# Kernel tuning notes

Hardware: AMD Instinct MI355X
Metric: run time of the kernel (lower is better)

## Reference

```python
import jax, jax.numpy as jnp
import numpy as np

B, C, H, W = 2, 1024, 64, 64
E, TOP_K = 8, 2
FFN = C  # ffn_dim = in_channels; hidden_dim = out_channels = in_channels


def setup_inputs() -> dict:
    key = jax.random.key(0)
    ks = jax.random.split(key, 5)
    s = 0.02
    return {
        "hidden_states": jax.random.normal(ks[0], (B, C, H, W), jnp.float32),
        "gate_w": jax.random.normal(ks[1], (E, C), jnp.float32) * s,   # torch Linear weight [out,in]
        "w1": jax.random.normal(ks[2], (E, FFN, C), jnp.float32) * s,
        "w2": jax.random.normal(ks[3], (E, C, FFN), jnp.float32) * s,
        "w3": jax.random.normal(ks[4], (E, FFN, C), jnp.float32) * s,
    }


def reference(hidden_states, gate_w, w1, w2, w3):
    b, c = hidden_states.shape[0], hidden_states.shape[1]
    space = hidden_states.shape[2:]
    # (B, C, H, W) -> (B, H, W, C) -> (T, C)
    x = jnp.transpose(hidden_states, (0, 2, 3, 1)).reshape(-1, c)

    # Router: softmax in float32, top-k, renormalize (matches torch)
    logits = x @ gate_w.T                                   # [T, E]
    probs = jax.nn.softmax(logits.astype(jnp.float32), axis=-1)
    rw, sel = jax.lax.top_k(probs, TOP_K)                   # [T, K]
    rw = rw / jnp.sum(rw, axis=-1, keepdims=True)
    rw = rw.astype(x.dtype)

    # Combine weights per expert: zero where expert not selected -> exact
    # equivalence with gather/scatter dispatch (full capacity, no drops).
    combine = jnp.sum(jax.nn.one_hot(sel, E, dtype=x.dtype) * rw[..., None], axis=1)  # [T, E]

    out = jnp.zeros_like(x)
    for e in range(E):  # small fixed expert loop
        h = jax.nn.gelu(x @ w1[e].T, approximate=False) * (x @ w3[e].T)  # SwiGLU-style [T, FFN]
        out = out + combine[:, e:e + 1] * (h @ w2[e].T)

    out = out.reshape(b, *space, c)
    return jnp.transpose(out, (0, 3, 1, 2))  # (B, C, H, W)
```

## Files before the change

### kernel.cpp

```cpp
#include <hip/hip_runtime.h>
#include <hip/hip_bf16.h>
#include <math.h>

#define BB 2
#define CC 1024
#define HH 64
#define WW 64
#define HWH (HH*WW)
#define TT (BB*HWH)
#define EE 8
#define FFN 1024
#define MAXTILES 71
#define HCAP (MAXTILES*256)

typedef __bf16 bf16x8 __attribute__((ext_vector_type(8)));
typedef __bf16 bf16x4 __attribute__((ext_vector_type(4)));
typedef float  f32x4  __attribute__((ext_vector_type(4)));

__device__ __forceinline__ void gl_lds16(const __bf16* g, __bf16* l) {
    __builtin_amdgcn_global_load_lds(
        (const __attribute__((address_space(1))) void*)g,
        (__attribute__((address_space(3))) void*)l, 16, 0, 0);
}

__device__ __forceinline__ void barrier_raw() {
    asm volatile("" ::: "memory");
    __builtin_amdgcn_s_barrier();
    asm volatile("" ::: "memory");
}

#define WAITV(N) asm volatile("s_waitcnt vmcnt(" #N ")" ::: "memory")
#define LGKM0()  asm volatile("s_waitcnt lgkmcnt(0)" ::: "memory")

#define MFMA16(ACC, AF, BF)                                                   \
    _Pragma("unroll") for (int m_ = 0; m_ < 4; ++m_)                          \
    _Pragma("unroll") for (int n_ = 0; n_ < 4; ++n_)                          \
        ACC[m_][n_] = __builtin_amdgcn_mfma_f32_16x16x32_bf16(                \
            AF[m_], BF[n_], ACC[m_][n_], 0, 0, 0);

#define CVB 12288
#define XPB 8192
#define RTB 512
__global__ __launch_bounds__(256) void k_prep(
    const float* __restrict__ hs, const float* __restrict__ gate_w,
    const float* __restrict__ w1, const float* __restrict__ w2,
    const float* __restrict__ w3,
    __bf16* __restrict__ w1b, __bf16* __restrict__ w2b,
    __bf16* __restrict__ w3b, __bf16* __restrict__ X,
    float* __restrict__ logP) {
    __shared__ float sm[2112];
    const int bid = blockIdx.x;
    const int tid = threadIdx.x;

    if (bid < CVB) {
        const float* s; __bf16* d; int lb = bid;
        if (lb < 4096)      { s = w1; d = w1b; }
        else if (lb < 8192) { s = w2; d = w2b; lb -= 4096; }
        else                { s = w3; d = w3b; lb -= 8192; }
        const size_t i = (size_t)lb * 2048 + (size_t)tid * 8;
        const f32x4 v0 = *(const f32x4*)&s[i];
        const f32x4 v1 = *(const f32x4*)&s[i + 4];
        bf16x8 o;
#pragma unroll
        for (int j = 0; j < 4; ++j) { o[j] = (__bf16)v0[j]; o[4 + j] = (__bf16)v1[j]; }
        *(bf16x8*)&d[i] = o;
    } else if (bid < CVB + XPB) {
        const int lb  = bid - CVB;
        const int hw0 = (lb & 127) * 32;
        const int c0  = ((lb >> 7) & 31) * 32;
        const int b   = lb >> 12;
        float (*tile)[33] = (float(*)[33])sm;
        const int tx = tid & 31, ty = tid >> 5;
        const float* src = hs + ((size_t)b * CC + c0) * HWH + hw0;
#pragma unroll
        for (int i = 0; i < 4; ++i)
            tile[ty + i * 8][tx] = src[(size_t)(ty + i * 8) * HWH + tx];
        __syncthreads();
        __bf16* dst = X + ((size_t)b * HWH + hw0) * CC + c0;
#pragma unroll
        for (int i = 0; i < 4; ++i) {
            const int hwl = ty + i * 8;
            dst[(size_t)hwl * CC + tx] = (__bf16)tile[tx][hwl];
        }
    } else {
        const int lb  = bid - (CVB + XPB);
        const int q   = lb & 3;
        const int t64 = lb >> 2;
        float* g = sm;
        for (int i = tid; i < 2048; i += 256)
            g[i] = gate_w[(size_t)(i >> 8) * CC + q * 256 + (i & 255)];
        __syncthreads();
        const int q2 = tid >> 6, tl = tid & 63;
        const int t  = t64 * 64 + tl;
        const int b  = t >> 12, hw = t & 4095;
        const float* xp = hs + (size_t)b * CC * HWH + hw;
        float l[EE];
#pragma unroll
        for (int e = 0; e < EE; ++e) l[e] = 0.0f;
        const int cbase = q * 256 + q2 * 64;
        for (int c2 = 0; c2 < 64; ++c2) {
            const float xv = xp[(size_t)(cbase + c2) * HWH];
#pragma unroll
            for (int e = 0; e < EE; ++e) l[e] += xv * g[e * 256 + q2 * 64 + c2];
        }
        float* dst = logP + ((size_t)(q * 4 + q2) * TT + t) * 8;
        f32x4 a, c;
#pragma unroll
        for (int e = 0; e < 4; ++e) { a[e] = l[e]; c[e] = l[4 + e]; }
        *(f32x4*)dst = a;
        *(f32x4*)&dst[4] = c;
    }
}

__global__ __launch_bounds__(256) void k_top2(const float* __restrict__ logP,
                                              int* __restrict__ cnt,
                                              int* __restrict__ idxl,
                                              int* __restrict__ tokE,
                                              int* __restrict__ tokP,
                                              float* __restrict__ tokW) {
    __shared__ int lcnt[EE], lbase[EE];
    const int tid = threadIdx.x;
    const int t   = blockIdx.x * 256 + tid;
    if (tid < EE) lcnt[tid] = 0;
    __syncthreads();

    float l[EE];
#pragma unroll
    for (int e = 0; e < EE; ++e) l[e] = 0.0f;
#pragma unroll
    for (int pq = 0; pq < 16; ++pq) {
        const float* src = logP + ((size_t)pq * TT + t) * 8;
        const f32x4 a = *(const f32x4*)src;
        const f32x4 c = *(const f32x4*)&src[4];
#pragma unroll
        for (int e = 0; e < 4; ++e) { l[e] += a[e]; l[4 + e] += c[e]; }
    }

    int e1 = 0; float v1 = l[0];
#pragma unroll
    for (int e = 1; e < EE; ++e) { if (l[e] > v1) { v1 = l[e]; e1 = e; } }
    int e2 = -1; float v2 = -1e30f;
#pragma unroll
    for (int e = 0; e < EE; ++e) { if (e != e1 && l[e] > v2) { v2 = l[e]; e2 = e; } }

    const float p2 = __expf(v2 - v1);
    const float rs = 1.0f / (1.0f + p2);

    const int m1 = atomicAdd(&lcnt[e1], 1);
    const int m2 = atomicAdd(&lcnt[e2], 1);
    __syncthreads();
    if (tid < EE) lbase[tid] = atomicAdd(&cnt[tid], lcnt[tid]);
    __syncthreads();
    const int p1pos = lbase[e1] + m1;
    const int p2pos = lbase[e2] + m2;

    idxl[e1 * TT + p1pos] = t;
    idxl[e2 * TT + p2pos] = t;
    tokE[t] = e1 | (e2 << 8);
    tokP[2 * t]     = p1pos;
    tokP[2 * t + 1] = p2pos;
    tokW[2 * t]     = rs;
    tokW[2 * t + 1] = p2 * rs;
}

__global__ void k_offsets(const int* __restrict__ cnt, int* __restrict__ off,
                          int* __restrict__ tileE, int* __restrict__ tileM,
                          int* __restrict__ nT) {
    if (threadIdx.x == 0) {
        int a = 0, n = 0;
        for (int e = 0; e < EE; ++e) {
            off[e] = a;
            const int mt = (cnt[e] + 255) >> 8;
            for (int m = 0; m < mt; ++m) { tileE[n] = e; tileM[n] = m * 256; ++n; }
            a += mt * 256;
        }
        nT[0] = n;
    }
}

__global__ __launch_bounds__(512, 2)
void k_gemm1(const __bf16* __restrict__ X, const __bf16* __restrict__ w1b,
             const __bf16* __restrict__ w3b, const int* __restrict__ cnt,
             const int* __restrict__ off, const int* __restrict__ idxl,
             const int* __restrict__ tileE, const int* __restrict__ tileM,
             const int* __restrict__ nT, __bf16* __restrict__ H) {
    if ((int)blockIdx.y >= nT[0]) return;
    const int e    = tileE[blockIdx.y];
    const int mt   = tileM[blockIdx.y];
    const int cntE = cnt[e];
    const int goff = off[e];
    const int n0   = blockIdx.x * 128;
    const __bf16* W1 = w1b + (size_t)e * FFN * CC;
    const __bf16* W3 = w3b + (size_t)e * FFN * CC;

    __shared__ __align__(16) __bf16 sA[4][256 * 32];
    __shared__ __align__(16) __bf16 sB1[4][128 * 32];
    __shared__ __align__(16) __bf16 sB3[4][128 * 32];

    const int tid  = threadIdx.x;
    const int lane = tid & 63, wave = tid >> 6;
    const int l15  = lane & 15, lq = (lane >> 4) & 3;
    const int wm   = (wave >> 1) * 64;
    const int wn   = (wave & 1) * 64;
    const int cs   = (lq ^ (l15 & 3)) * 8;
    const int r_l  = tid >> 2;
    const int csw8 = ((tid & 3) ^ (r_l & 3)) * 8;

    int p0 = mt + r_l;        if (p0 > cntE - 1) p0 = cntE - 1;
    int p1 = mt + 128 + r_l;  if (p1 > cntE - 1) p1 = cntE - 1;
    const __bf16* gA0 = X + (size_t)idxl[e * TT + p0] * CC + csw8;
    const __bf16* gA1 = X + (size_t)idxl[e * TT + p1] * CC + csw8;
    const __bf16* gW1 = W1 + (size_t)(n0 + r_l) * CC + csw8;
    const __bf16* gW3 = W3 + (size_t)(n0 + r_l) * CC + csw8;

    const int aoff = (wm + l15) * 32 + cs;
    const int boff = (wn + l15) * 32 + cs;
    const int dA   = wave * 512;

    f32x4 acc1[4][4] = {};
    f32x4 acc3[4][4] = {};

#define STG1A(S, KT) do { const int kb_ = (KT) * 32;                          \
        gl_lds16(gA0 + kb_, &sA[S][dA]);                                      \
        gl_lds16(gA1 + kb_, &sA[S][4096 + dA]); } while (0)
#define STG1B(S, KT) do { const int kb_ = (KT) * 32;                          \
        gl_lds16(gW1 + kb_, &sB1[S][dA]);                                     \
        gl_lds16(gW3 + kb_, &sB3[S][dA]); } while (0)

    STG1A(0, 0); STG1B(0, 0);
    STG1A(1, 1); STG1B(1, 1);
    STG1A(2, 2); STG1B(2, 2);
    WAITV(8);
    barrier_raw();

#define TILE1(KT, S, PREF, WN) do {                                           \
    bf16x8 af_[4], bf_[4];                                                    \
    _Pragma("unroll") for (int i_ = 0; i_ < 4; ++i_) {                        \
        af_[i_] = *(const bf16x8*)&sA[S][aoff + i_ * 512];                    \
        bf_[i_] = *(const bf16x8*)&sB1[S][boff + i_ * 512];                   \
    }                                                                         \
    if (PREF) STG1A((S + 3) & 3, (KT) + 3);                                   \
    barrier_raw();                                                            \
    LGKM0();                                                                  \
    __builtin_amdgcn_s_setprio(1);                                            \
    MFMA16(acc1, af_, bf_);                                                   \
    __builtin_amdgcn_s_setprio(0);                                            \
    barrier_raw();                                                            \
    _Pragma("unroll") for (int i_ = 0; i_ < 4; ++i_)                          \
        bf_[i_] = *(const bf16x8*)&sB3[S][boff + i_ * 512];                   \
    if (PREF) STG1B((S + 3) & 3, (KT) + 3);                                   \
    barrier_raw();                                                            \
    LGKM0();                                                                  \
    __builtin_amdgcn_s_setprio(1);                                            \
    MFMA16(acc3, af_, bf_);                                                   \
    __builtin_amdgcn_s_setprio(0);                                            \
    WAITV(WN);                                                                \
    barrier_raw();                                                            \
} while (0)

    for (int k4 = 0; k4 < 28; k4 += 4) {
        TILE1(k4 + 0, 0, 1, 8);
        TILE1(k4 + 1, 1, 1, 8);
        TILE1(k4 + 2, 2, 1, 8);
        TILE1(k4 + 3, 3, 1, 8);
    }
    TILE1(28, 0, 1, 8);
    TILE1(29, 1, 0, 4);
    TILE1(30, 2, 0, 0);
    TILE1(31, 3, 0, 63);

#pragma unroll
    for (int m = 0; m < 4; ++m) {
        const int gb = goff + mt + wm + m * 16 + lq * 4;
#pragma unroll
        for (int n = 0; n < 4; ++n) {
            const int nb = n0 + wn + n * 16 + l15;
#pragma unroll
            for (int r = 0; r < 4; ++r) {
                const float a  = acc1[m][n][r];
                const float c  = acc3[m][n][r];
                const float ge = 0.5f * a * (1.0f + erff(a * 0.70710678118654752f));
                H[(size_t)(gb + r) * FFN + nb] = (__bf16)(ge * c);
            }
        }
    }
}

__global__ __launch_bounds__(512, 2)
void k_gemm2(const __bf16* __restrict__ H, const __bf16* __restrict__ w2b,
             const int* __restrict__ off, const int* __restrict__ tileE,
             const int* __restrict__ tileM, const int* __restrict__ nT,
             __bf16* __restrict__ Z) {
    if ((int)blockIdx.y >= nT[0]) return;
    const int e    = tileE[blockIdx.y];
    const int mt   = tileM[blockIdx.y];
    const int goff = off[e];
    const int n0   = blockIdx.x * 256;
    const __bf16* W2 = w2b + (size_t)e * CC * FFN;
    const __bf16* Ar = H + (size_t)(goff + mt) * FFN;

    __shared__ __align__(16) __bf16 sA[4][256 * 32];
    __shared__ __align__(16) __bf16 sB[4][256 * 32];

    const int tid  = threadIdx.x;
    const int lane = tid & 63, wave = tid >> 6;
    const int l15  = lane & 15, lq = (lane >> 4) & 3;
    const int wm   = (wave & 1) * 128;
    const int wn   = (wave >> 1) * 64;
    const int cs   = (lq ^ (l15 & 3)) * 8;
    const int r_l  = tid >> 2;
    const int csw8 = ((tid & 3) ^ (r_l & 3)) * 8;

    const __bf16* gA0 = Ar + (size_t)r_l * FFN + csw8;
    const __bf16* gA1 = Ar + (size_t)(128 + r_l) * FFN + csw8;
    const __bf16* gB0 = W2 + (size_t)(n0 + r_l) * FFN + csw8;
    const __bf16* gB1 = W2 + (size_t)(n0 + 128 + r_l) * FFN + csw8;

    const int aoff = (wm + l15) * 32 + cs;
    const int boff = (wn + l15) * 32 + cs;
    const int dA   = wave * 512;

    f32x4 accL[4][4] = {};
    f32x4 accH[4][4] = {};

#define STG2A(S, KT) do { const int kb_ = (KT) * 32;                          \
        gl_lds16(gA0 + kb_, &sA[S][dA]);                                      \
        gl_lds16(gA1 + kb_, &sA[S][4096 + dA]); } while (0)
#define STG2B(S, KT) do { const int kb_ = (KT) * 32;                          \
        gl_lds16(gB0 + kb_, &sB[S][dA]);                                      \
        gl_lds16(gB1 + kb_, &sB[S][4096 + dA]); } while (0)

    STG2A(0, 0); STG2B(0, 0);
    STG2A(1, 1); STG2B(1, 1);
    STG2A(2, 2); STG2B(2, 2);
    WAITV(8);
    barrier_raw();

#define TILE2(KT, S, PREF, WN) do {                                           \
    bf16x8 af_[4], bf_[4];                                                    \
    _Pragma("unroll") for (int i_ = 0; i_ < 4; ++i_) {                        \
        af_[i_] = *(const bf16x8*)&sA[S][aoff + i_ * 512];                    \
        bf_[i_] = *(const bf16x8*)&sB[S][boff + i_ * 512];                    \
    }                                                                         \
    if (PREF) STG2A((S + 3) & 3, (KT) + 3);                                   \
    barrier_raw();                                                            \
    LGKM0();                                                                  \
    __builtin_amdgcn_s_setprio(1);                                            \
    MFMA16(accL, af_, bf_);                                                   \
    __builtin_amdgcn_s_setprio(0);                                            \
    barrier_raw();                                                            \
    _Pragma("unroll") for (int i_ = 0; i_ < 4; ++i_)                          \
        af_[i_] = *(const bf16x8*)&sA[S][aoff + 2048 + i_ * 512];             \
    if (PREF) STG2B((S + 3) & 3, (KT) + 3);                                   \
    barrier_raw();                                                            \
    LGKM0();                                                                  \
    __builtin_amdgcn_s_setprio(1);                                            \
    MFMA16(accH, af_, bf_);                                                   \
    __builtin_amdgcn_s_setprio(0);                                            \
    WAITV(WN);                                                                \
    barrier_raw();                                                            \
} while (0)

    for (int k4 = 0; k4 < 28; k4 += 4) {
        TILE2(k4 + 0, 0, 1, 8);
        TILE2(k4 + 1, 1, 1, 8);
        TILE2(k4 + 2, 2, 1, 8);
        TILE2(k4 + 3, 3, 1, 8);
    }
    TILE2(28, 0, 1, 8);
    TILE2(29, 1, 0, 4);
    TILE2(30, 2, 0, 0);
    TILE2(31, 3, 0, 63);

#pragma unroll
    for (int m = 0; m < 4; ++m) {
#pragma unroll
        for (int n = 0; n < 4; ++n) {
            const int nb = n0 + wn + n * 16 + l15;
#pragma unroll
            for (int r = 0; r < 4; ++r) {
                Z[(size_t)(goff + mt + wm + m * 16 + lq * 4 + r) * CC + nb] =
                    (__bf16)accL[m][n][r];
                Z[(size_t)(goff + mt + wm + 64 + m * 16 + lq * 4 + r) * CC + nb] =
                    (__bf16)accH[m][n][r];
            }
        }
    }
}

__global__ __launch_bounds__(256) void k_combine(const __bf16* __restrict__ Z,
                                                 const int* __restrict__ off,
                                                 const int* __restrict__ tokE,
                                                 const int* __restrict__ tokP,
                                                 const float* __restrict__ tokW,
                                                 float* __restrict__ out) {
    __shared__ float tile[32][33];
    const int t0 = blockIdx.x * 32;
    const int c0 = blockIdx.y * 32;
    const int tx = threadIdx.x & 31;
    const int ty = threadIdx.x >> 5;

#pragma unroll
    for (int i = 0; i < 4; ++i) {
        const int tl = ty + 8 * i;
        const int t  = t0 + tl;
        const int ee = tokE[t];
        const int e1 = ee & 0xff, e2 = ee >> 8;
        const int r1 = off[e1] + tokP[2 * t];
        const int r2 = off[e2] + tokP[2 * t + 1];
        const float v = tokW[2 * t]     * (float)Z[(size_t)r1 * CC + c0 + tx]
                      + tokW[2 * t + 1] * (float)Z[(size_t)r2 * CC + c0 + tx];
        tile[tl][tx] = v;
    }
    __syncthreads();

    const int b   = t0 >> 12;
    const int hw0 = t0 & 4095;
#pragma unroll
    for (int i = 0; i < 4; ++i) {
        const int cl = ty + 8 * i;
        out[(size_t)b * CC * HWH + (size_t)(c0 + cl) * HWH + hw0 + tx] = tile[tx][cl];
    }
}

extern "C" void kernel_launch(void* const* d_in, const int* in_sizes, int n_in,
                              void* d_out, int out_size, void* d_ws, size_t ws_size,
                              hipStream_t stream) {
    const float* hs     = (const float*)d_in[0];
    const float* gate_w = (const float*)d_in[1];
    const float* w1     = (const float*)d_in[2];
    const float* w2     = (const float*)d_in[3];
    const float* w3     = (const float*)d_in[4];
    float* out = (float*)d_out;

    const size_t WSZ = (size_t)EE * FFN * CC * 2;
    char* ws = (char*)d_ws;
    __bf16* w2b  = (__bf16*)ws;
    __bf16* w1b  = (__bf16*)(ws + WSZ);
    __bf16* w3b  = (__bf16*)(ws + 2 * WSZ);
    __bf16* X    = (__bf16*)(ws + 3 * WSZ);
    __bf16* Zbuf = (__bf16*)(ws + WSZ);
    __bf16* Hbuf = (__bf16*)(ws + 4 * WSZ);
    float*  logP = (float*)Hbuf;
    char* p = ws + 4 * WSZ + (size_t)HCAP * FFN * 2;
    int*   idxl  = (int*)p;           p += (size_t)EE * TT * 4;
    int*   tokE  = (int*)p;           p += (size_t)TT * 4;
    int*   tokP  = (int*)p;           p += (size_t)2 * TT * 4;
    float* tokW  = (float*)p;         p += (size_t)2 * TT * 4;
    int*   cnt   = (int*)p;           p += 256;
    int*   off   = (int*)p;           p += 256;
    int*   tileE = (int*)p;           p += MAXTILES * 4;
    int*   tileM = (int*)p;           p += MAXTILES * 4;
    int*   nT    = (int*)p;

    hipMemsetAsync(cnt, 0, EE * sizeof(int), stream);

    k_prep<<<CVB + XPB + RTB, 256, 0, stream>>>(
        hs, gate_w, w1, w2, w3, w1b, w2b, w3b, X, logP);
    k_top2<<<TT / 256, 256, 0, stream>>>(logP, cnt, idxl, tokE, tokP, tokW);
    k_offsets<<<1, 64, 0, stream>>>(cnt, off, tileE, tileM, nT);

    k_gemm1<<<dim3(FFN / 128, MAXTILES), 512, 0, stream>>>(
        X, w1b, w3b, cnt, off, idxl, tileE, tileM, nT, Hbuf);
    k_gemm2<<<dim3(CC / 256, MAXTILES), 512, 0, stream>>>(
        Hbuf, w2b, off, tileE, tileM, nT, Zbuf);
    k_combine<<<dim3(TT / 32, CC / 32), 256, 0, stream>>>(
        Zbuf, off, tokE, tokP, tokW, out);
}
```

Measured before the change: 383.5 us.

## Restructure MoE GEMM kernels to double-buffered BK=64 with 128x64 wave tiles

Both expert GEMM kernels move from a 4-stage BK=32 pipeline to a 2-stage double buffer that covers 64 of K per stage. Each wave now owns a 128x64 output subtile, with 8x4 accumulators and interleaved W1/W3 columns in gemm1. The LDS swizzle pattern changes and sched_barrier hints are added. Launch bounds drop to one block per CU to free registers for the larger accumulator set, at the cost of lower occupancy and less latency hiding.

```diff
diff --git a/kernel.cpp b/kernel.cpp
--- a/kernel.cpp
+++ b/kernel.cpp
@@ -14,7 +14,6 @@
 #define HCAP (MAXTILES*256)
 
 typedef __bf16 bf16x8 __attribute__((ext_vector_type(8)));
-typedef __bf16 bf16x4 __attribute__((ext_vector_type(4)));
 typedef float  f32x4  __attribute__((ext_vector_type(4)));
 
 __device__ __forceinline__ void gl_lds16(const __bf16* g, __bf16* l) {
@@ -31,12 +30,9 @@
 
 #define WAITV(N) asm volatile("s_waitcnt vmcnt(" #N ")" ::: "memory")
 #define LGKM0()  asm volatile("s_waitcnt lgkmcnt(0)" ::: "memory")
-
-#define MFMA16(ACC, AF, BF)                                                   \
-    _Pragma("unroll") for (int m_ = 0; m_ < 4; ++m_)                          \
-    _Pragma("unroll") for (int n_ = 0; n_ < 4; ++n_)                          \
-        ACC[m_][n_] = __builtin_amdgcn_mfma_f32_16x16x32_bf16(                \
-            AF[m_], BF[n_], ACC[m_][n_], 0, 0, 0);
+#define SCHED0() __builtin_amdgcn_sched_barrier(0)
+#define PRIO1()  __builtin_amdgcn_s_setprio(1)
+#define PRIO0()  __builtin_amdgcn_s_setprio(0)
 
 #define CVB 12288
 #define XPB 8192
@@ -178,7 +174,7 @@
     }
 }
 
-__global__ __launch_bounds__(512, 2)
+__global__ __launch_bounds__(512, 1)
 void k_gemm1(const __bf16* __restrict__ X, const __bf16* __restrict__ w1b,
              const __bf16* __restrict__ w3b, const int* __restrict__ cnt,
              const int* __restrict__ off, const int* __restrict__ idxl,
@@ -193,100 +189,114 @@
     const __bf16* W1 = w1b + (size_t)e * FFN * CC;
     const __bf16* W3 = w3b + (size_t)e * FFN * CC;
 
-    __shared__ __align__(16) __bf16 sA[4][256 * 32];
-    __shared__ __align__(16) __bf16 sB1[4][128 * 32];
-    __shared__ __align__(16) __bf16 sB3[4][128 * 32];
+    __shared__ __align__(16) __bf16 sA[2][2][256 * 32];
+    __shared__ __align__(16) __bf16 sB[2][2][256 * 32];
 
     const int tid  = threadIdx.x;
     const int lane = tid & 63, wave = tid >> 6;
-    const int l15  = lane & 15, lq = (lane >> 4) & 3;
-    const int wm   = (wave >> 1) * 64;
-    const int wn   = (wave & 1) * 64;
-    const int cs   = (lq ^ (l15 & 3)) * 8;
-    const int r_l  = tid >> 2;
-    const int csw8 = ((tid & 3) ^ (r_l & 3)) * 8;
-
-    int p0 = mt + r_l;        if (p0 > cntE - 1) p0 = cntE - 1;
-    int p1 = mt + 128 + r_l;  if (p1 > cntE - 1) p1 = cntE - 1;
-    const __bf16* gA0 = X + (size_t)idxl[e * TT + p0] * CC + csw8;
-    const __bf16* gA1 = X + (size_t)idxl[e * TT + p1] * CC + csw8;
-    const __bf16* gW1 = W1 + (size_t)(n0 + r_l) * CC + csw8;
-    const __bf16* gW3 = W3 + (size_t)(n0 + r_l) * CC + csw8;
-
-    const int aoff = (wm + l15) * 32 + cs;
-    const int boff = (wn + l15) * 32 + cs;
-    const int dA   = wave * 512;
-
-    f32x4 acc1[4][4] = {};
-    f32x4 acc3[4][4] = {};
-
-#define STG1A(S, KT) do { const int kb_ = (KT) * 32;                          \
-        gl_lds16(gA0 + kb_, &sA[S][dA]);                                      \
-        gl_lds16(gA1 + kb_, &sA[S][4096 + dA]); } while (0)
-#define STG1B(S, KT) do { const int kb_ = (KT) * 32;                          \
-        gl_lds16(gW1 + kb_, &sB1[S][dA]);                                     \
-        gl_lds16(gW3 + kb_, &sB3[S][dA]); } while (0)
-
-    STG1A(0, 0); STG1B(0, 0);
-    STG1A(1, 1); STG1B(1, 1);
-    STG1A(2, 2); STG1B(2, 2);
-    WAITV(8);
+    const int l15  = lane & 15, lq = lane >> 4;
+    const int wm   = wave & 1;
+    const int q    = wave >> 1;
+    const int rsw  = (lq ^ ((l15 >> 1) & 3)) * 8;
+
+    const int rl  = lane >> 2;
+    const int csw = ((lane & 3) ^ ((rl >> 1) & 3)) * 8;
+
+    int pr0 = mt + wave * 32 + rl;       if (pr0 > cntE - 1) pr0 = cntE - 1;
+    int pr1 = mt + wave * 32 + 16 + rl;  if (pr1 > cntE - 1) pr1 = cntE - 1;
+    const __bf16* gA0 = X + (size_t)idxl[e * TT + pr0] * CC + csw;
+    const __bf16* gA1 = X + (size_t)idxl[e * TT + pr1] * CC + csw;
+    const __bf16* WB = (wave & 1) ? W3 : W1;
+    const __bf16* gB0 = WB + (size_t)(n0 + q * 32 + rl) * CC + csw;
+    const __bf16* gB1 = WB + (size_t)(n0 + q * 32 + 16 + rl) * CC + csw;
+
+    const int st0  = wave * 1024;
+    const int aoff = (wm * 128 + l15) * 32 + rsw;
+    const int boff = (q * 64 + l15) * 32 + rsw;
+
+    f32x4 acc[8][4] = {};
+
+#define G1_STGA(S, KS, KB) do {                                               \
+    gl_lds16(gA0 + (KB) + (KS) * 32, &sA[S][KS][st0]);                        \
+    gl_lds16(gA1 + (KB) + (KS) * 32, &sA[S][KS][st0 + 512]); } while (0)
+#define G1_STGB(S, KS, KB) do {                                               \
+    gl_lds16(gB0 + (KB) + (KS) * 32, &sB[S][KS][st0]);                        \
+    gl_lds16(gB1 + (KB) + (KS) * 32, &sB[S][KS][st0 + 512]); } while (0)
+#define G1_LDA(DST, S, KS, MF0)                                               \
+    _Pragma("unroll") for (int mf_ = 0; mf_ < 4; ++mf_)                       \
+        DST[mf_] = *(const bf16x8*)&sA[S][KS][aoff + (MF0 + mf_) * 512];
+#define G1_LDB(DST, S, KS)                                                    \
+    _Pragma("unroll") for (int nf_ = 0; nf_ < 4; ++nf_)                       \
+        DST[nf_] = *(const bf16x8*)&sB[S][KS][boff + nf_ * 512];
+#define G1_MM(M0, AF, BF)                                                     \
+    _Pragma("unroll") for (int m_ = 0; m_ < 4; ++m_)                          \
+    _Pragma("unroll") for (int n_ = 0; n_ < 4; ++n_)                          \
+        acc[M0 + m_][n_] = __builtin_amdgcn_mfma_f32_16x16x32_bf16(           \
+            AF[m_], BF[n_], acc[M0 + m_][n_], 0, 0, 0);
+
+#define G1_TILE(S, KB, STG, LAST) do {                                        \
+    bf16x8 af[4], bv[4];                                                      \
+                                 \
+    G1_LDA(af, S, 0, 0); G1_LDB(bv, S, 0);                                    \
+    if (STG) G1_STGA((S) ^ 1, 0, KB);                                         \
+    barrier_raw(); LGKM0(); SCHED0();                                         \
+    PRIO1(); G1_MM(0, af, bv); PRIO0(); barrier_raw();                        \
+                                               \
+    G1_LDA(af, S, 0, 4);                                                      \
+    if (STG) G1_STGB((S) ^ 1, 0, KB);                                         \
+    if (LAST) { WAITV(0); } else { WAITV(4); }                                \
+    barrier_raw(); LGKM0(); SCHED0();                                         \
+    PRIO1(); G1_MM(4, af, bv); PRIO0(); barrier_raw();                        \
+                                 \
+    G1_LDA(af, S, 1, 0); G1_LDB(bv, S, 1);                                    \
+    if (STG) G1_STGA((S) ^ 1, 1, KB);                                         \
+    barrier_raw(); LGKM0(); SCHED0();                                         \
+    PRIO1(); G1_MM(0, af, bv); PRIO0(); barrier_raw();                        \
+                                               \
+    G1_LDA(af, S, 1, 4);                                                      \
+    if (STG) G1_STGB((S) ^ 1, 1, KB);                                         \
+    if (!LAST) { WAITV(4); }                                                  \
+    barrier_raw(); LGKM0(); SCHED0();                                         \
+    PRIO1(); G1_MM(4, af, bv); PRIO0(); barrier_raw();                        \
+} while (0)
+
+    G1_STGA(0, 0, 0); G1_STGB(0, 0, 0); G1_STGA(0, 1, 0); G1_STGB(0, 1, 0);
+    WAITV(0);
     barrier_raw();
 
-#define TILE1(KT, S, PREF, WN) do {                                           \
-    bf16x8 af_[4], bf_[4];                                                    \
-    _Pragma("unroll") for (int i_ = 0; i_ < 4; ++i_) {                        \
-        af_[i_] = *(const bf16x8*)&sA[S][aoff + i_ * 512];                    \
-        bf_[i_] = *(const bf16x8*)&sB1[S][boff + i_ * 512];                   \
-    }                                                                         \
-    if (PREF) STG1A((S + 3) & 3, (KT) + 3);                                   \
-    barrier_raw();                                                            \
-    LGKM0();                                                                  \
-    __builtin_amdgcn_s_setprio(1);                                            \
-    MFMA16(acc1, af_, bf_);                                                   \
-    __builtin_amdgcn_s_setprio(0);                                            \
-    barrier_raw();                                                            \
-    _Pragma("unroll") for (int i_ = 0; i_ < 4; ++i_)                          \
-        bf_[i_] = *(const bf16x8*)&sB3[S][boff + i_ * 512];                   \
-    if (PREF) STG1B((S + 3) & 3, (KT) + 3);                                   \
-    barrier_raw();                                                            \
-    LGKM0();                                                                  \
-    __builtin_amdgcn_s_setprio(1);                                            \
-    MFMA16(acc3, af_, bf_);                                                   \
-    __builtin_amdgcn_s_setprio(0);                                            \
-    WAITV(WN);                                                                \
-    barrier_raw();                                                            \
-} while (0)
-
-    for (int k4 = 0; k4 < 28; k4 += 4) {
-        TILE1(k4 + 0, 0, 1, 8);
-        TILE1(k4 + 1, 1, 1, 8);
-        TILE1(k4 + 2, 2, 1, 8);
-        TILE1(k4 + 3, 3, 1, 8);
-    }
-    TILE1(28, 0, 1, 8);
-    TILE1(29, 1, 0, 4);
-    TILE1(30, 2, 0, 0);
-    TILE1(31, 3, 0, 63);
-
-#pragma unroll
-    for (int m = 0; m < 4; ++m) {
-        const int gb = goff + mt + wm + m * 16 + lq * 4;
-#pragma unroll
-        for (int n = 0; n < 4; ++n) {
-            const int nb = n0 + wn + n * 16 + l15;
+    int kb = 64;
+    for (int it = 0; it < 7; ++it) {
+        G1_TILE(0, kb, 1, 0); kb += 64;
+        G1_TILE(1, kb, 1, 0); kb += 64;
+    }
+    G1_TILE(0, kb, 1, 0);
+    G1_TILE(1, 0, 0, 1);
+
+#undef G1_STGA
+#undef G1_STGB
+#undef G1_LDA
+#undef G1_LDB
+#undef G1_MM
+#undef G1_TILE
+
+#pragma unroll
+    for (int mf = 0; mf < 8; ++mf) {
+        const int gr = goff + mt + wm * 128 + mf * 16 + lq * 4;
+#pragma unroll
+        for (int jp = 0; jp < 2; ++jp) {
+            const int col = n0 + q * 32 + jp * 16 + l15;
 #pragma unroll
             for (int r = 0; r < 4; ++r) {
-                const float a  = acc1[m][n][r];
-                const float c  = acc3[m][n][r];
+                const float a  = acc[mf][jp][r];
+                const float c  = acc[mf][jp + 2][r];
                 const float ge = 0.5f * a * (1.0f + erff(a * 0.70710678118654752f));
-                H[(size_t)(gb + r) * FFN + nb] = (__bf16)(ge * c);
+                H[(size_t)(gr + r) * FFN + col] = (__bf16)(ge * c);
             }
         }
     }
 }
 
-__global__ __launch_bounds__(512, 2)
+__global__ __launch_bounds__(512, 1)
 void k_gemm2(const __bf16* __restrict__ H, const __bf16* __restrict__ w2b,
              const int* __restrict__ off, const int* __restrict__ tileE,
              const int* __restrict__ tileM, const int* __restrict__ nT,
@@ -299,91 +309,97 @@
     const __bf16* W2 = w2b + (size_t)e * CC * FFN;
     const __bf16* Ar = H + (size_t)(goff + mt) * FFN;
 
-    __shared__ __align__(16) __bf16 sA[4][256 * 32];
-    __shared__ __align__(16) __bf16 sB[4][256 * 32];
+    __shared__ __align__(16) __bf16 sA[2][2][256 * 32];
+    __shared__ __align__(16) __bf16 sB[2][2][256 * 32];
 
     const int tid  = threadIdx.x;
     const int lane = tid & 63, wave = tid >> 6;
-    const int l15  = lane & 15, lq = (lane >> 4) & 3;
-    const int wm   = (wave & 1) * 128;
-    const int wn   = (wave >> 1) * 64;
-    const int cs   = (lq ^ (l15 & 3)) * 8;
-    const int r_l  = tid >> 2;
-    const int csw8 = ((tid & 3) ^ (r_l & 3)) * 8;
-
-    const __bf16* gA0 = Ar + (size_t)r_l * FFN + csw8;
-    const __bf16* gA1 = Ar + (size_t)(128 + r_l) * FFN + csw8;
-    const __bf16* gB0 = W2 + (size_t)(n0 + r_l) * FFN + csw8;
-    const __bf16* gB1 = W2 + (size_t)(n0 + 128 + r_l) * FFN + csw8;
-
-    const int aoff = (wm + l15) * 32 + cs;
-    const int boff = (wn + l15) * 32 + cs;
-    const int dA   = wave * 512;
-
-    f32x4 accL[4][4] = {};
-    f32x4 accH[4][4] = {};
-
-#define STG2A(S, KT) do { const int kb_ = (KT) * 32;                          \
-        gl_lds16(gA0 + kb_, &sA[S][dA]);                                      \
-        gl_lds16(gA1 + kb_, &sA[S][4096 + dA]); } while (0)
-#define STG2B(S, KT) do { const int kb_ = (KT) * 32;                          \
-        gl_lds16(gB0 + kb_, &sB[S][dA]);                                      \
-        gl_lds16(gB1 + kb_, &sB[S][4096 + dA]); } while (0)
-
-    STG2A(0, 0); STG2B(0, 0);
-    STG2A(1, 1); STG2B(1, 1);
-    STG2A(2, 2); STG2B(2, 2);
-    WAITV(8);
+    const int l15  = lane & 15, lq = lane >> 4;
+    const int wm   = wave & 1;
+    const int q    = wave >> 1;
+    const int rsw  = (lq ^ ((l15 >> 1) & 3)) * 8;
+    const int rl   = lane >> 2;
+    const int csw  = ((lane & 3) ^ ((rl >> 1) & 3)) * 8;
+
+    const __bf16* gA0 = Ar + (size_t)(wave * 32 + rl) * FFN + csw;
+    const __bf16* gA1 = Ar + (size_t)(wave * 32 + 16 + rl) * FFN + csw;
+    const __bf16* gB0 = W2 + (size_t)(n0 + wave * 32 + rl) * FFN + csw;
+    const __bf16* gB1 = W2 + (size_t)(n0 + wave * 32 + 16 + rl) * FFN + csw;
+
+    const int st0  = wave * 1024;
+    const int aoff = (wm * 128 + l15) * 32 + rsw;
+    const int boff = (q * 64 + l15) * 32 + rsw;
+
+    f32x4 acc[8][4] = {};
+
+#define G2_STGA(S, KS, KB) do {                                               \
+    gl_lds16(gA0 + (KB) + (KS) * 32, &sA[S][KS][st0]);                        \
+    gl_lds16(gA1 + (KB) + (KS) * 32, &sA[S][KS][st0 + 512]); } while (0)
+#define G2_STGB(S, KS, KB) do {                                               \
+    gl_lds16(gB0 + (KB) + (KS) * 32, &sB[S][KS][st0]);                        \
+    gl_lds16(gB1 + (KB) + (KS) * 32, &sB[S][KS][st0 + 512]); } while (0)
+#define G2_LDA(DST, S, KS, MF0)                                               \
+    _Pragma("unroll") for (int mf_ = 0; mf_ < 4; ++mf_)                       \
+        DST[mf_] = *(const bf16x8*)&sA[S][KS][aoff + (MF0 + mf_) * 512];
+#define G2_LDB(DST, S, KS)                                                    \
+    _Pragma("unroll") for (int nf_ = 0; nf_ < 4; ++nf_)                       \
+        DST[nf_] = *(const bf16x8*)&sB[S][KS][boff + nf_ * 512];
+#define G2_MM(M0, AF, BF)                                                     \
+    _Pragma("unroll") for (int m_ = 0; m_ < 4; ++m_)                          \
+    _Pragma("unroll") for (int n_ = 0; n_ < 4; ++n_)                          \
+        acc[M0 + m_][n_] = __builtin_amdgcn_mfma_f32_16x16x32_bf16(           \
+            AF[m_], BF[n_], acc[M0 + m_][n_], 0, 0, 0);
+
+#define G2_TILE(S, KB, STG, LAST) do {                                        \
+    bf16x8 af[4], bv[4];                                                      \
+    G2_LDA(af, S, 0, 0); G2_LDB(bv, S, 0);                                    \
+    if (STG) G2_STGA((S) ^ 1, 0, KB);                                         \
+    barrier_raw(); LGKM0(); SCHED0();                                         \
+    PRIO1(); G2_MM(0, af, bv); PRIO0(); barrier_raw();                        \
+    G2_LDA(af, S, 0, 4);                                                      \
+    if (STG) G2_STGB((S) ^ 1, 0, KB);                                         \
+    if (LAST) { WAITV(0); } else { WAITV(4); }                                \
+    barrier_raw(); LGKM0(); SCHED0();                                         \
+    PRIO1(); G2_MM(4, af, bv); PRIO0(); barrier_raw();                        \
+    G2_LDA(af, S, 1, 0); G2_LDB(bv, S, 1);                                    \
+    if (STG) G2_STGA((S) ^ 1, 1, KB);                                         \
+    barrier_raw(); LGKM0(); SCHED0();                                         \
+    PRIO1(); G2_MM(0, af, bv); PRIO0(); barrier_raw();                        \
+    G2_LDA(af, S, 1, 4);                                                      \
+    if (STG) G2_STGB((S) ^ 1, 1, KB);                                         \
+    if (!LAST) { WAITV(4); }                                                  \
+    barrier_raw(); LGKM0(); SCHED0();                                         \
+    PRIO1(); G2_MM(4, af, bv); PRIO0(); barrier_raw();                        \
+} while (0)
+
+    G2_STGA(0, 0, 0); G2_STGB(0, 0, 0); G2_STGA(0, 1, 0); G2_STGB(0, 1, 0);
+    WAITV(0);
     barrier_raw();
 
-#define TILE2(KT, S, PREF, WN) do {                                           \
-    bf16x8 af_[4], bf_[4];                                                    \
-    _Pragma("unroll") for (int i_ = 0; i_ < 4; ++i_) {                        \
-        af_[i_] = *(const bf16x8*)&sA[S][aoff + i_ * 512];                    \
-        bf_[i_] = *(const bf16x8*)&sB[S][boff + i_ * 512];                    \
-    }                                                                         \
-    if (PREF) STG2A((S + 3) & 3, (KT) + 3);                                   \
-    barrier_raw();                                                            \
-    LGKM0();                                                                  \
-    __builtin_amdgcn_s_setprio(1);                                            \
-    MFMA16(accL, af_, bf_);                                                   \
-    __builtin_amdgcn_s_setprio(0);                                            \
-    barrier_raw();                                                            \
-    _Pragma("unroll") for (int i_ = 0; i_ < 4; ++i_)                          \
-        af_[i_] = *(const bf16x8*)&sA[S][aoff + 2048 + i_ * 512];             \
-    if (PREF) STG2B((S + 3) & 3, (KT) + 3);                                   \
-    barrier_raw();                                                            \
-    LGKM0();                                                                  \
-    __builtin_amdgcn_s_setprio(1);                                            \
-    MFMA16(accH, af_, bf_);                                                   \
-    __builtin_amdgcn_s_setprio(0);                                            \
-    WAITV(WN);                                                                \
-    barrier_raw();                                                            \
-} while (0)
-
-    for (int k4 = 0; k4 < 28; k4 += 4) {
-        TILE2(k4 + 0, 0, 1, 8);
-        TILE2(k4 + 1, 1, 1, 8);
-        TILE2(k4 + 2, 2, 1, 8);
-        TILE2(k4 + 3, 3, 1, 8);
-    }
-    TILE2(28, 0, 1, 8);
-    TILE2(29, 1, 0, 4);
-    TILE2(30, 2, 0, 0);
-    TILE2(31, 3, 0, 63);
-
-#pragma unroll
-    for (int m = 0; m < 4; ++m) {
-#pragma unroll
-        for (int n = 0; n < 4; ++n) {
-            const int nb = n0 + wn + n * 16 + l15;
-#pragma unroll
-            for (int r = 0; r < 4; ++r) {
-                Z[(size_t)(goff + mt + wm + m * 16 + lq * 4 + r) * CC + nb] =
-                    (__bf16)accL[m][n][r];
-                Z[(size_t)(goff + mt + wm + 64 + m * 16 + lq * 4 + r) * CC + nb] =
-                    (__bf16)accH[m][n][r];
-            }
+    int kb = 64;
+    for (int it = 0; it < 7; ++it) {
+        G2_TILE(0, kb, 1, 0); kb += 64;
+        G2_TILE(1, kb, 1, 0); kb += 64;
+    }
+    G2_TILE(0, kb, 1, 0);
+    G2_TILE(1, 0, 0, 1);
+
+#undef G2_STGA
+#undef G2_STGB
+#undef G2_LDA
+#undef G2_LDB
+#undef G2_MM
+#undef G2_TILE
+
+#pragma unroll
+    for (int mf = 0; mf < 8; ++mf) {
+        const int gr = goff + mt + wm * 128 + mf * 16 + lq * 4;
+#pragma unroll
+        for (int nf = 0; nf < 4; ++nf) {
+            const int col = n0 + q * 64 + nf * 16 + l15;
+#pragma unroll
+            for (int r = 0; r < 4; ++r)
+                Z[(size_t)(gr + r) * CC + col] = (__bf16)acc[mf][nf][r];
         }
     }
 }
```

Result: no change. 380.9 us (-0.7%).
